# Kernel tuning notes

Hardware: AMD Instinct MI355X
Metric: run time of the kernel (lower is better)

The kernel has to match this reference:

```python
import jax, jax.numpy as jnp
import numpy as np

# Bahdanau additive attention (eval mode: dropout is identity):
#   fac1 = W @ k        [B, d, S]
#   fac2 = U @ q        [B, d, S]
#   s    = v^T tanh(fac1 + fac2)   [B, 1, S]
#   attn = softmax(s, axis=-1)

B, D, S = 32, 1024, 2048


def setup_inputs() -> dict:
    key = jax.random.key(0)
    kq, kk, kv, kW, kU = jax.random.split(key, 5)
    scale = 1.0 / np.sqrt(D)
    return {
        "q": jax.random.normal(kq, (B, D, S), dtype=jnp.float32),
        "k": jax.random.normal(kk, (B, D, S), dtype=jnp.float32),
        "v": jax.random.normal(kv, (B, D, 1), dtype=jnp.float32),
        "W": jax.random.normal(kW, (D, D), dtype=jnp.float32) * scale,
        "U": jax.random.normal(kU, (D, D), dtype=jnp.float32) * scale,
    }


def reference(q, k, v, W, U):
    # projections: [d,e] x [b,e,s] -> [b,d,s]
    fac1 = jnp.einsum("de,bes->bds", W, k)
    fac2 = jnp.einsum("de,bes->bds", U, q)
    e = jnp.tanh(fac1 + fac2)            # [B, D, S]
    s = jnp.einsum("bdo,bds->bos", v, e)  # [B, 1, S]
    attn = jax.nn.softmax(s, axis=-1)     # softmax over sequence
    return attn
```

## Files before the change

### kernel.cpp

```cpp
#include <hip/hip_runtime.h>

#define D_ 1024
#define S_ 2048
#define B_ 32
#define BM 256
#define BN 128
#define NKT 32
#define NPH 64

typedef __attribute__((ext_vector_type(8))) _Float16 f16x8;
typedef __attribute__((ext_vector_type(16))) float f32x16;

__device__ __forceinline__ void async_ld16(const void* g, void* l) {
  __builtin_amdgcn_global_load_lds(
      (const __attribute__((address_space(1))) void*)g,
      (__attribute__((address_space(3))) void*)l, 16, 0, 0);
}

__global__ void prep_kernel(const float* __restrict__ W, const float* __restrict__ U,
                            _Float16* __restrict__ wf, _Float16* __restrict__ uf) {
  int t = blockIdx.x * blockDim.x + threadIdx.x;
  const float* src = blockIdx.y ? U : W;
  _Float16* dst = blockIdx.y ? uf : wf;

  int tile = t >> 11;
  int g    = t & 2047;
  int top  = g >> 6;
  int ks = top >> 3, wr = (top >> 2) & 1, fm = top & 3;
  int lane = g & 63, l31 = lane & 31, lhi = lane >> 5;
  int row   = wr * 128 + fm * 32 + l31;
  int chunk = ks * 2 + lhi;
  int d = (tile >> 4) * 256 + row;
  int e = (tile & 15) * 64 + chunk * 8;

  const float* p = src + (size_t)d * D_ + e;
  f16x8 hv;
#pragma unroll
  for (int j = 0; j < 8; ++j) hv[j] = (_Float16)p[j];
  *(f16x8*)(dst + (size_t)t * 8) = hv;
}

__global__ void kqprep_kernel(const float* __restrict__ kten, const float* __restrict__ qten,
                              _Float16* __restrict__ bfmt) {
  size_t t = (size_t)blockIdx.x * 256 + threadIdx.x;
  int g    = (int)(t & 1023);
  int tile = (int)(t >> 10);
  int st   = tile & 15;
  int ktt  = (tile >> 4) & 15;
  int half = (tile >> 8) & 1;
  int b    = tile >> 9;
  int l31 = g & 31, clh = (g >> 5) & 1, w2 = (g >> 6) & 3, cks = (g >> 8) & 3;
  int n = w2 * 32 + l31;
  int c = cks * 2 + clh;
  int e = ktt * 64 + c * 8;
  int s = st * 128 + n;

  const float* src = (half ? qten : kten) + (size_t)b * (D_ * S_) + (size_t)e * S_ + s;
  f16x8 hv;
#pragma unroll
  for (int j = 0; j < 8; ++j) hv[j] = (_Float16)src[(size_t)j * S_];
  *(f16x8*)(bfmt + t * 8) = hv;
}

__global__ void __launch_bounds__(256, 2)
gemm_kernel(const float* __restrict__ v,
            const _Float16* __restrict__ wf, const _Float16* __restrict__ uf,
            const _Float16* __restrict__ bfmt,
            float* __restrict__ partials) {
  __shared__ __align__(16) _Float16 Af[3][BM * 32];
  __shared__ __align__(16) _Float16 Bf[3][BN * 32];
  __shared__ float vbuf[BM];
  __shared__ float red[2][BN];

  const int tid  = threadIdx.x;
  const int lane = tid & 63;
  const int wid  = tid >> 6;
  const int wr   = wid >> 1;
  const int wc   = wid & 1;

  int bid  = blockIdx.x;
  int g    = ((bid >> 5) << 3) | (bid & 7);
  int dblk = (bid >> 3) & 3;
  int st   = g & 15;
  int b    = g >> 4;
  int s0   = st * BN;

  vbuf[tid] = v[(size_t)b * D_ + dblk * BM + tid];
  __syncthreads();

  f32x16 acc[4][2];
#pragma unroll
  for (int i = 0; i < 4; ++i)
#pragma unroll
    for (int j = 0; j < 2; ++j)
#pragma unroll
      for (int r = 0; r < 16; ++r) acc[i][j][r] = 0.0f;

#define PH_FENCE asm volatile("" ::: "memory")
#define WAIT6 asm volatile("s_waitcnt vmcnt(6)" ::: "memory")
#define WAIT0 asm volatile("s_waitcnt vmcnt(0)" ::: "memory")

#define GLLH(h_, bi_) do {                                                     \
    const int kt_ = (h_) >> 1, hh_ = (h_) & 1;                                 \
    const int half_ = kt_ >> 4, ktt_ = kt_ & 15;                               \
    const _Float16* at_ = (half_ ? uf : wf)                                    \
        + (size_t)(dblk * 16 + ktt_) * 16384 + (size_t)hh_ * 8192;             \
    const _Float16* bt_ = bfmt                                                 \
        + ((size_t)(((b * 2 + half_) * 16 + ktt_) * 16 + st)) * 8192           \
        + (size_t)hh_ * 4096;                                                  \
    _Pragma("unroll")                                                          \
    for (int i = 0; i < 4; ++i)                                                \
      async_ld16(at_ + (size_t)(tid + i * 256) * 8,                            \
                 &Af[bi_][(size_t)(tid + i * 256) * 8]);                       \
    _Pragma("unroll")                                                          \
    for (int i = 0; i < 2; ++i)                                                \
      async_ld16(bt_ + (size_t)(tid + i * 256) * 8,                            \
                 &Bf[bi_][(size_t)(tid + i * 256) * 8]);                       \
  } while (0)

#define PHASE(bi_, ISSUE, WAITC) do {                                          \
    PH_FENCE;                                                                  \
    f16x8 a0_[4], a1_[4], b0_[2], b1_[2];                                      \
    _Pragma("unroll")                                                          \
    for (int fm = 0; fm < 4; ++fm) {                                           \
      a0_[fm] = *(const f16x8*)&Af[bi_][(size_t)((((wr * 4 + fm)) * 64 + lane)) * 8]; \
      a1_[fm] = *(const f16x8*)&Af[bi_][(size_t)(((8 + wr * 4 + fm) * 64 + lane)) * 8]; \
    }                                                                          \
    _Pragma("unroll")                                                          \
    for (int fn = 0; fn < 2; ++fn) {                                           \
      b0_[fn] = *(const f16x8*)&Bf[bi_][(size_t)((((wc * 2 + fn)) * 64 + lane)) * 8]; \
      b1_[fn] = *(const f16x8*)&Bf[bi_][(size_t)(((4 + wc * 2 + fn) * 64 + lane)) * 8]; \
    }                                                                          \
    ISSUE;                                                                     \
    __builtin_amdgcn_s_barrier();                                              \
    asm volatile("s_waitcnt lgkmcnt(0)" ::: "memory");                         \
    __builtin_amdgcn_sched_barrier(0);                                         \
    __builtin_amdgcn_s_setprio(1);                                             \
    _Pragma("unroll")                                                          \
    for (int fm = 0; fm < 4; ++fm)                                             \
      _Pragma("unroll")                                                        \
      for (int fn = 0; fn < 2; ++fn)                                           \
        acc[fm][fn] = __builtin_amdgcn_mfma_f32_32x32x16_f16(a0_[fm], b0_[fn], acc[fm][fn], 0, 0, 0); \
    _Pragma("unroll")                                                          \
    for (int fm = 0; fm < 4; ++fm)                                             \
      _Pragma("unroll")                                                        \
      for (int fn = 0; fn < 2; ++fn)                                           \
        acc[fm][fn] = __builtin_amdgcn_mfma_f32_32x32x16_f16(a1_[fm], b1_[fn], acc[fm][fn], 0, 0, 0); \
    __builtin_amdgcn_s_setprio(0);                                             \
    WAITC;                                                                     \
    __builtin_amdgcn_s_barrier();                                              \
    __builtin_amdgcn_sched_barrier(0);                                         \
  } while (0)

  PH_FENCE;
  GLLH(0, 0);
  GLLH(1, 1);
  WAIT6;
  __builtin_amdgcn_s_barrier();
  __builtin_amdgcn_sched_barrier(0);

  for (int m = 0; m < 20; ++m) {
    const int h = 3 * m;
    PHASE(0, GLLH(h + 2, 2), WAIT6);
    PHASE(1, GLLH(h + 3, 0), WAIT6);
    PHASE(2, GLLH(h + 4, 1), WAIT6);
  }
  PHASE(0, GLLH(62, 2), WAIT6);
  PHASE(1, GLLH(63, 0), WAIT6);
  PHASE(2, , WAIT0);
  PHASE(0, , );

#undef PHASE
#undef GLLH
#undef WAIT0
#undef WAIT6
#undef PH_FENCE

  float psum[2] = {0.f, 0.f};
#pragma unroll
  for (int fm = 0; fm < 4; ++fm)
#pragma unroll
    for (int fn = 0; fn < 2; ++fn)
#pragma unroll
      for (int r = 0; r < 16; ++r) {
        int row = wr * 128 + fm * 32 + (r & 3) + 8 * (r >> 2) + 4 * (lane >> 5);
        float x  = acc[fm][fn][r];
        float th = 1.0f - 2.0f / (__expf(2.0f * x) + 1.0f);
        psum[fn] += vbuf[row] * th;
      }
#pragma unroll
  for (int fn = 0; fn < 2; ++fn) psum[fn] += __shfl_xor(psum[fn], 32);
  if (lane < 32) {
    red[wr][wc * 64 + lane]      = psum[0];
    red[wr][wc * 64 + 32 + lane] = psum[1];
  }
  __syncthreads();
  if (tid < BN) {
    float val = red[0][tid] + red[1][tid];
    partials[(size_t)(dblk * B_ + b) * S_ + s0 + tid] = val;
  }
}

__global__ void __launch_bounds__(512, 2)
gemm_fb_kernel(const float* __restrict__ kten, const float* __restrict__ qten,
               const float* __restrict__ v,
               const _Float16* __restrict__ wf, const _Float16* __restrict__ uf,
               float* __restrict__ partials) {
  __shared__ __align__(16) _Float16 Af[2][256 * 64];
  __shared__ __align__(16) _Float16 Bf[2][256 * 64];
  __shared__ float vbuf[256];
  __shared__ float red[2][256];

  const int tid  = threadIdx.x;
  const int lane = tid & 63;
  const int wid  = tid >> 6;
  const int wr   = wid >> 2;
  const int wc   = wid & 3;

  int bid  = blockIdx.x;
  int g    = ((bid >> 5) << 3) | (bid & 7);
  int dblk = (bid >> 3) & 3;
  int st   = g & 7;
  int b    = g >> 3;
  int s0   = st * 256;

  if (tid < 256) vbuf[tid] = v[(size_t)b * D_ + dblk * 256 + tid];

  f32x16 acc[4][2];
#pragma unroll
  for (int i = 0; i < 4; ++i)
#pragma unroll
    for (int j = 0; j < 2; ++j)
#pragma unroll
      for (int r = 0; r < 16; ++r) acc[i][j][r] = 0.0f;

  const int nB = tid & 255;
  const int kq = tid >> 8;

#define PH_FENCE_F asm volatile("" ::: "memory")
#define PH_BAR_F __builtin_amdgcn_s_barrier()

#define GLLA_F(ktn, buf, part) do {                                            \
    const int half_ = (ktn) >> 4, ktt_ = (ktn) & 15;                           \
    const _Float16* at_ = (half_ ? uf : wf) + (size_t)(dblk * 16 + ktt_) * 16384; \
    async_ld16(at_ + (size_t)(tid + (part) * 1024) * 8,                        \
               &Af[buf][(size_t)(tid + (part) * 1024) * 8]);                   \
    async_ld16(at_ + (size_t)(tid + (part) * 1024 + 512) * 8,                  \
               &Af[buf][(size_t)(tid + (part) * 1024 + 512) * 8]);             \
  } while (0)

#define LOADB_F(ktn, xv, h) do {                                               \
    const int half_ = (ktn) >> 4, ktt_ = (ktn) & 15;                           \
    const float* col_ = (half_ ? qten : kten) + (size_t)b * (D_ * S_)          \
                        + (size_t)(ktt_ * 64) * S_ + s0 + nB                   \
                        + (size_t)(kq * 32) * S_;                              \
    _Pragma("unroll")                                                          \
    for (int j = 16 * (h); j < 16 * (h) + 16; ++j) xv[j] = col_[(size_t)j * S_]; \
  } while (0)

#define CVTWRITE_F(xv, buf) do {                                               \
    _Pragma("unroll")                                                          \
    for (int cl = 0; cl < 4; ++cl) {                                           \
      f16x8 hv_;                                                               \
      _Pragma("unroll")                                                        \
      for (int w = 0; w < 8; ++w) hv_[w] = (_Float16)xv[cl * 8 + w];           \
      int c_ = kq * 4 + cl, cks_ = c_ >> 1, clh_ = c_ & 1;                     \
      int gnl_ = ((cks_ * 8 + (nB >> 6) * 2 + ((nB >> 5) & 1)) << 6)           \
                 | (clh_ << 5) | (nB & 31);                                    \
      *(f16x8*)&Bf[buf][(size_t)gnl_ * 8] = hv_;                               \
    }                                                                          \
  } while (0)

#define COMPUTE_PHASE_F(cur_, ks_) do {                                        \
    f16x8 af_[4], bf_[2];                                                      \
    _Pragma("unroll")                                                          \
    for (int fm = 0; fm < 4; ++fm)                                             \
      af_[fm] = *(const f16x8*)&Af[cur_][(size_t)(((ks_) * 8 + wr * 4 + fm) * 64 + lane) * 8]; \
    _Pragma("unroll")                                                          \
    for (int fn = 0; fn < 2; ++fn)                                             \
      bf_[fn] = *(const f16x8*)&Bf[cur_][(size_t)(((ks_) * 8 + wc * 2 + fn) * 64 + lane) * 8]; \
    __builtin_amdgcn_s_setprio(1);                                             \
    _Pragma("unroll")                                                          \
    for (int fm = 0; fm < 4; ++fm)                                             \
      _Pragma("unroll")                                                        \
      for (int fn = 0; fn < 2; ++fn)                                           \
        acc[fm][fn] = __builtin_amdgcn_mfma_f32_32x32x16_f16(af_[fm], bf_[fn], acc[fm][fn], 0, 0, 0); \
    __builtin_amdgcn_s_setprio(0);                                             \
  } while (0)

#define STEP_F(kt_, cur_, xvC_, xvN_) do {                                     \
    const int nxt_ = (cur_) ^ 1;                                               \
    PH_FENCE_F; GLLA_F((kt_) + 1, nxt_, 0); COMPUTE_PHASE_F(cur_, 0); PH_BAR_F;\
    PH_FENCE_F; GLLA_F((kt_) + 1, nxt_, 1); COMPUTE_PHASE_F(cur_, 1); PH_BAR_F;\
    PH_FENCE_F; LOADB_F((kt_) + 2, xvN_, 0); COMPUTE_PHASE_F(cur_, 2); PH_BAR_F;\
    PH_FENCE_F; LOADB_F((kt_) + 2, xvN_, 1); CVTWRITE_F(xvC_, nxt_);           \
              COMPUTE_PHASE_F(cur_, 3);                                        \
    asm volatile("s_waitcnt vmcnt(32) lgkmcnt(0)" ::: "memory");               \
    PH_BAR_F;                                                                  \
    __builtin_amdgcn_sched_barrier(0);                                         \
  } while (0)

  float xvA[32], xvB[32];
  LOADB_F(0, xvA, 0); LOADB_F(0, xvA, 1);
  GLLA_F(0, 0, 0);    GLLA_F(0, 0, 1);
  LOADB_F(1, xvB, 0); LOADB_F(1, xvB, 1);
  CVTWRITE_F(xvA, 0);
  __syncthreads();

  for (int it = 0; it < 15; ++it) {
    STEP_F(2 * it,     0, xvB, xvA);
    STEP_F(2 * it + 1, 1, xvA, xvB);
  }

  PH_FENCE_F; GLLA_F(31, 1, 0); COMPUTE_PHASE_F(0, 0); PH_BAR_F;
  PH_FENCE_F; GLLA_F(31, 1, 1); COMPUTE_PHASE_F(0, 1); PH_BAR_F;
  PH_FENCE_F; COMPUTE_PHASE_F(0, 2); PH_BAR_F;
  PH_FENCE_F; CVTWRITE_F(xvB, 1); COMPUTE_PHASE_F(0, 3);
  __syncthreads();
  COMPUTE_PHASE_F(1, 0); COMPUTE_PHASE_F(1, 1); COMPUTE_PHASE_F(1, 2); COMPUTE_PHASE_F(1, 3);

#undef STEP_F
#undef COMPUTE_PHASE_F
#undef CVTWRITE_F
#undef LOADB_F
#undef GLLA_F
#undef PH_BAR_F
#undef PH_FENCE_F

  float psum[2] = {0.f, 0.f};
#pragma unroll
  for (int fm = 0; fm < 4; ++fm)
#pragma unroll
    for (int fn = 0; fn < 2; ++fn)
#pragma unroll
      for (int r = 0; r < 16; ++r) {
        int row = wr * 128 + fm * 32 + (r & 3) + 8 * (r >> 2) + 4 * (lane >> 5);
        float x  = acc[fm][fn][r];
        float th = 1.0f - 2.0f / (__expf(2.0f * x) + 1.0f);
        psum[fn] += vbuf[row] * th;
      }
#pragma unroll
  for (int fn = 0; fn < 2; ++fn) psum[fn] += __shfl_xor(psum[fn], 32);
  if (lane < 32) {
    red[wr][wc * 64 + lane]      = psum[0];
    red[wr][wc * 64 + 32 + lane] = psum[1];
  }
  __syncthreads();
  if (tid < 256) {
    float val = red[0][tid] + red[1][tid];
    partials[(size_t)(dblk * B_ + b) * S_ + s0 + tid] = val;
  }
}

__global__ void softmax_kernel(const float* __restrict__ partials, float* __restrict__ out) {
  __shared__ float logit[S_];
  __shared__ float wred[2][4];
  int b = blockIdx.x, tid = threadIdx.x;
  int lane = tid & 63, wid = tid >> 6;
  float lmax = -1e30f;
  for (int i = tid; i < S_; i += 256) {
    float acc = 0.f;
#pragma unroll
    for (int d = 0; d < 4; ++d) acc += partials[(size_t)(d * B_ + b) * S_ + i];
    logit[i] = acc;
    lmax = fmaxf(lmax, acc);
  }
#pragma unroll
  for (int o = 32; o; o >>= 1) lmax = fmaxf(lmax, __shfl_xor(lmax, o));
  if (lane == 0) wred[0][wid] = lmax;
  __syncthreads();
  float m = fmaxf(fmaxf(wred[0][0], wred[0][1]), fmaxf(wred[0][2], wred[0][3]));
  float lsum = 0.f;
  for (int i = tid; i < S_; i += 256) {
    float ex = __expf(logit[i] - m);
    logit[i] = ex;
    lsum += ex;
  }
#pragma unroll
  for (int o = 32; o; o >>= 1) lsum += __shfl_xor(lsum, o);
  if (lane == 0) wred[1][wid] = lsum;
  __syncthreads();
  float tot = wred[1][0] + wred[1][1] + wred[1][2] + wred[1][3];
  float inv = 1.0f / tot;
  for (int i = tid; i < S_; i += 256) out[(size_t)b * S_ + i] = logit[i] * inv;
}

extern "C" void kernel_launch(void* const* d_in, const int* in_sizes, int n_in,
                              void* d_out, int out_size, void* d_ws, size_t ws_size,
                              hipStream_t stream) {
  const float* q = (const float*)d_in[0];
  const float* k = (const float*)d_in[1];
  const float* v = (const float*)d_in[2];
  const float* W = (const float*)d_in[3];
  const float* U = (const float*)d_in[4];

  _Float16* wf = (_Float16*)d_ws;
  _Float16* uf = wf + (size_t)D_ * D_;
  float* partials = (float*)(uf + (size_t)D_ * D_);
  _Float16* bfmt = (_Float16*)((char*)d_ws + 5242880);
  const size_t NEED = 5242880ull + 268435456ull;

  prep_kernel<<<dim3(512, 2), 256, 0, stream>>>(W, U, wf, uf);
  if (ws_size >= NEED) {
    kqprep_kernel<<<dim3(65536), 256, 0, stream>>>(k, q, bfmt);
    gemm_kernel<<<dim3(2048), 256, 0, stream>>>(v, wf, uf, bfmt, partials);
  } else {
    gemm_fb_kernel<<<dim3(1024), 512, 0, stream>>>(k, q, v, wf, uf, partials);
  }
  softmax_kernel<<<dim3(B_), 256, 0, stream>>>(partials, (float*)d_out);
}
```

Before: 426.9 us.

## Load MFMA fragments directly from global memory into registers, dropping LDS staging

Removes the triple-buffered LDS pipeline (global_load_lds plus barriers) and instead has each wave load its A/B f16 fragments straight from pre-swizzled global memory into registers, with a four-deep register rotation for software pipelining. This is meant to eliminate LDS traffic and block-wide barriers. The cost is that A and B tiles are no longer shared across waves through LDS, so every wave fetches its own copy from L2/global. Register pressure also rises from holding four fragment sets in flight.

```diff
diff --git a/kernel.cpp b/kernel.cpp
--- a/kernel.cpp
+++ b/kernel.cpp
@@ -5,8 +5,6 @@
 #define B_ 32
 #define BM 256
 #define BN 128
-#define NKT 32
-#define NPH 64
 
 typedef __attribute__((ext_vector_type(8))) _Float16 f16x8;
 typedef __attribute__((ext_vector_type(16))) float f32x16;
@@ -67,8 +65,6 @@
             const _Float16* __restrict__ wf, const _Float16* __restrict__ uf,
             const _Float16* __restrict__ bfmt,
             float* __restrict__ partials) {
-  __shared__ __align__(16) _Float16 Af[3][BM * 32];
-  __shared__ __align__(16) _Float16 Bf[3][BN * 32];
   __shared__ float vbuf[BM];
   __shared__ float red[2][BN];
 
@@ -88,6 +84,11 @@
   vbuf[tid] = v[(size_t)b * D_ + dblk * BM + tid];
   __syncthreads();
 
+  const int aoffw = dblk * 262144 + wr * 2048 + lane * 8;
+  const int boffw = wc * 1024 + lane * 8;
+  const _Float16* bbk = bfmt + (size_t)(b * 2 + 0) * 2097152 + (size_t)st * 8192;
+  const _Float16* bbq = bfmt + (size_t)(b * 2 + 1) * 2097152 + (size_t)st * 8192;
+
   f32x16 acc[4][2];
 #pragma unroll
   for (int i = 0; i < 4; ++i)
@@ -96,85 +97,48 @@
 #pragma unroll
       for (int r = 0; r < 16; ++r) acc[i][j][r] = 0.0f;
 
-#define PH_FENCE asm volatile("" ::: "memory")
-#define WAIT6 asm volatile("s_waitcnt vmcnt(6)" ::: "memory")
-#define WAIT0 asm volatile("s_waitcnt vmcnt(0)" ::: "memory")
-
-#define GLLH(h_, bi_) do {                                                     \
-    const int kt_ = (h_) >> 1, hh_ = (h_) & 1;                                 \
-    const int half_ = kt_ >> 4, ktt_ = kt_ & 15;                               \
-    const _Float16* at_ = (half_ ? uf : wf)                                    \
-        + (size_t)(dblk * 16 + ktt_) * 16384 + (size_t)hh_ * 8192;             \
-    const _Float16* bt_ = bfmt                                                 \
-        + ((size_t)(((b * 2 + half_) * 16 + ktt_) * 16 + st)) * 8192           \
-        + (size_t)hh_ * 4096;                                                  \
-    _Pragma("unroll")                                                          \
-    for (int i = 0; i < 4; ++i)                                                \
-      async_ld16(at_ + (size_t)(tid + i * 256) * 8,                            \
-                 &Af[bi_][(size_t)(tid + i * 256) * 8]);                       \
-    _Pragma("unroll")                                                          \
-    for (int i = 0; i < 2; ++i)                                                \
-      async_ld16(bt_ + (size_t)(tid + i * 256) * 8,                            \
-                 &Bf[bi_][(size_t)(tid + i * 256) * 8]);                       \
-  } while (0)
-
-#define PHASE(bi_, ISSUE, WAITC) do {                                          \
-    PH_FENCE;                                                                  \
-    f16x8 a0_[4], a1_[4], b0_[2], b1_[2];                                      \
-    _Pragma("unroll")                                                          \
-    for (int fm = 0; fm < 4; ++fm) {                                           \
-      a0_[fm] = *(const f16x8*)&Af[bi_][(size_t)((((wr * 4 + fm)) * 64 + lane)) * 8]; \
-      a1_[fm] = *(const f16x8*)&Af[bi_][(size_t)(((8 + wr * 4 + fm) * 64 + lane)) * 8]; \
-    }                                                                          \
-    _Pragma("unroll")                                                          \
-    for (int fn = 0; fn < 2; ++fn) {                                           \
-      b0_[fn] = *(const f16x8*)&Bf[bi_][(size_t)((((wc * 2 + fn)) * 64 + lane)) * 8]; \
-      b1_[fn] = *(const f16x8*)&Bf[bi_][(size_t)(((4 + wc * 2 + fn) * 64 + lane)) * 8]; \
-    }                                                                          \
-    ISSUE;                                                                     \
-    __builtin_amdgcn_s_barrier();                                              \
-    asm volatile("s_waitcnt lgkmcnt(0)" ::: "memory");                         \
-    __builtin_amdgcn_sched_barrier(0);                                         \
-    __builtin_amdgcn_s_setprio(1);                                             \
+#define LOADSET(FA, FB, s_) do {                                               \
+    const int sv_ = (s_);                                                      \
+    const int ks_ = sv_ & 3, ktt_ = (sv_ >> 2) & 15;                           \
+    const _Float16* ab_ = (sv_ >= 64 ? uf : wf)                                \
+        + (size_t)((sv_ & 63) * 4096 + aoffw);                                 \
+    const _Float16* bb_ = (sv_ >= 64 ? bbq : bbk)                              \
+        + (size_t)(ktt_ * 131072 + ks_ * 2048 + boffw);                        \
+    _Pragma("unroll")                                                          \
+    for (int fm = 0; fm < 4; ++fm) FA[fm] = *(const f16x8*)(ab_ + fm * 512);   \
+    _Pragma("unroll")                                                          \
+    for (int fn = 0; fn < 2; ++fn) FB[fn] = *(const f16x8*)(bb_ + fn * 512);   \
+  } while (0)
+
+#define COMPSET(FA, FB) do {                                                   \
     _Pragma("unroll")                                                          \
     for (int fm = 0; fm < 4; ++fm)                                             \
       _Pragma("unroll")                                                        \
       for (int fn = 0; fn < 2; ++fn)                                           \
-        acc[fm][fn] = __builtin_amdgcn_mfma_f32_32x32x16_f16(a0_[fm], b0_[fn], acc[fm][fn], 0, 0, 0); \
-    _Pragma("unroll")                                                          \
-    for (int fm = 0; fm < 4; ++fm)                                             \
-      _Pragma("unroll")                                                        \
-      for (int fn = 0; fn < 2; ++fn)                                           \
-        acc[fm][fn] = __builtin_amdgcn_mfma_f32_32x32x16_f16(a1_[fm], b1_[fn], acc[fm][fn], 0, 0, 0); \
-    __builtin_amdgcn_s_setprio(0);                                             \
-    WAITC;                                                                     \
-    __builtin_amdgcn_s_barrier();                                              \
-    __builtin_amdgcn_sched_barrier(0);                                         \
-  } while (0)
-
-  PH_FENCE;
-  GLLH(0, 0);
-  GLLH(1, 1);
-  WAIT6;
-  __builtin_amdgcn_s_barrier();
-  __builtin_amdgcn_sched_barrier(0);
-
-  for (int m = 0; m < 20; ++m) {
-    const int h = 3 * m;
-    PHASE(0, GLLH(h + 2, 2), WAIT6);
-    PHASE(1, GLLH(h + 3, 0), WAIT6);
-    PHASE(2, GLLH(h + 4, 1), WAIT6);
-  }
-  PHASE(0, GLLH(62, 2), WAIT6);
-  PHASE(1, GLLH(63, 0), WAIT6);
-  PHASE(2, , WAIT0);
-  PHASE(0, , );
-
-#undef PHASE
-#undef GLLH
-#undef WAIT0
-#undef WAIT6
-#undef PH_FENCE
+        acc[fm][fn] = __builtin_amdgcn_mfma_f32_32x32x16_f16(FA[fm], FB[fn], acc[fm][fn], 0, 0, 0); \
+  } while (0)
+
+  f16x8 fa0[4], fb0[2], fa1[4], fb1[2], fa2[4], fb2[2], fa3[4], fb3[2];
+
+  LOADSET(fa0, fb0, 0);
+  LOADSET(fa1, fb1, 1);
+  LOADSET(fa2, fb2, 2);
+
+  for (int i = 0; i < 31; ++i) {
+    const int s4 = i * 4;
+    LOADSET(fa3, fb3, s4 + 3); COMPSET(fa0, fb0);
+    LOADSET(fa0, fb0, s4 + 4); COMPSET(fa1, fb1);
+    LOADSET(fa1, fb1, s4 + 5); COMPSET(fa2, fb2);
+    LOADSET(fa2, fb2, s4 + 6); COMPSET(fa3, fb3);
+  }
+  LOADSET(fa3, fb3, 127);
+  COMPSET(fa0, fb0);
+  COMPSET(fa1, fb1);
+  COMPSET(fa2, fb2);
+  COMPSET(fa3, fb3);
+
+#undef COMPSET
+#undef LOADSET
 
   float psum[2] = {0.f, 0.f};
 #pragma unroll
```

After: 472.4 us. 1.11x slower.
